# Kernel tuning notes

Hardware: AMD Instinct MI355X
Metric: run time of the kernel (lower is better)

## Reference

```python
import jax, jax.numpy as jnp
import numpy as np

N_HEADS = 4
HEAD_DIM = 128
FMAP_H, FMAP_W = 32, 32
IN_DIM = 512
BATCH = 16


def setup_inputs() -> dict:
    key = jax.random.key(0)
    k1, k2, k3, k4 = jax.random.split(key, 4)
    scale = HEAD_DIM ** (-0.5)
    x = jax.random.normal(k1, (BATCH, IN_DIM, FMAP_H, FMAP_W), dtype=jnp.float32)
    # 1x1 conv weight producing q,k,v stacked along output channels
    conv_w = jax.random.normal(k2, (3 * N_HEADS * HEAD_DIM, IN_DIM), dtype=jnp.float32) * (IN_DIM ** -0.5)
    pos_h = jax.random.normal(k3, (FMAP_H, HEAD_DIM), dtype=jnp.float32) * scale
    pos_w = jax.random.normal(k4, (FMAP_W, HEAD_DIM), dtype=jnp.float32) * scale
    return {"x": x, "conv_w": conv_w, "pos_h": pos_h, "pos_w": pos_w}


def reference(x, conv_w, pos_h, pos_w):
    B, C, H, W = x.shape
    hw = H * W
    scale = HEAD_DIM ** (-0.5)
    # 1x1 conv == pointwise linear over channels
    qkv = jnp.einsum('bchw,oc->bohw', x, conv_w)               # [B, 3*nh*hd, H, W]
    qkv = qkv.reshape(B, 3, N_HEADS, HEAD_DIM, hw)             # chunk + per-head split
    q = jnp.swapaxes(qkv[:, 0], -1, -2) * scale                # [B, nh, hw, hd]
    k = jnp.swapaxes(qkv[:, 1], -1, -2)
    v = jnp.swapaxes(qkv[:, 2], -1, -2)
    # absolute positional embedding: h[i,:]+w[j,:] flattened over positions
    emb = (pos_h[:, None, :] + pos_w[None, :, :]).reshape(hw, HEAD_DIM)
    sim = jnp.einsum('bhid,bhjd->bhij', q, k) + jnp.einsum('bhid,jd->bhij', q, emb)
    attn = jax.nn.softmax(sim, axis=-1)
    out = jnp.einsum('bhij,bhjd->bhid', attn, v)               # [B, nh, hw, hd]
    out = jnp.swapaxes(out, -1, -2)                            # [B, nh, hd, hw]
    return out.reshape(B, N_HEADS * HEAD_DIM, hw // N_HEADS, N_HEADS)
```

## Files before the change

### kernel.cpp

```cpp
#include <hip/hip_runtime.h>

#define NB 16
#define NH 4
#define HD 128
#define HW 1024
#define CIN 512

typedef short s16x8 __attribute__((ext_vector_type(8)));
typedef short s16x4 __attribute__((ext_vector_type(4)));
typedef float f32x4 __attribute__((ext_vector_type(4)));

static __device__ __forceinline__ short f2bf(float f) {
    union { float f; unsigned u; } v; v.f = f;
    unsigned r = v.u + 0x7fffu + ((v.u >> 16) & 1u);
    return (short)(r >> 16);
}

__global__ __launch_bounds__(256) void prep_xw(
    const float* __restrict__ x, const float* __restrict__ w,
    short* __restrict__ xT, short* __restrict__ Wb)
{
    int blk = blockIdx.x;
    if (blk < NB * 16 * 32) {
        int b = blk >> 9, rem = blk & 511;
        int ct = rem >> 5, pt = rem & 31;
        __shared__ float tile[32][33];
        int tc = threadIdx.x >> 5;
        int tp = threadIdx.x & 31;
        const float* xb = x + ((size_t)b * CIN + ct * 32) * HW + pt * 32;
        #pragma unroll
        for (int i = 0; i < 4; i++)
            tile[tc + i * 8][tp] = xb[(size_t)(tc + i * 8) * HW + tp];
        __syncthreads();
        int p = threadIdx.x >> 3, cq = threadIdx.x & 7;
        short* xo = xT + ((size_t)b * HW + pt * 32 + p) * CIN + ct * 32 + cq * 4;
        s16x4 o4 = { f2bf(tile[cq * 4 + 0][p]), f2bf(tile[cq * 4 + 1][p]),
                     f2bf(tile[cq * 4 + 2][p]), f2bf(tile[cq * 4 + 3][p]) };
        *reinterpret_cast<s16x4*>(xo) = o4;
    } else {
        int wb = blk - NB * 16 * 32;
        size_t base = (size_t)wb * 1024 + threadIdx.x * 4;
        const float4 v = *reinterpret_cast<const float4*>(w + base);
        s16x4 o4 = { f2bf(v.x), f2bf(v.y), f2bf(v.z), f2bf(v.w) };
        *reinterpret_cast<s16x4*>(Wb + base) = o4;
    }
}

__global__ __launch_bounds__(256, 3) void qkv_proj(
    const short* __restrict__ xT, const short* __restrict__ Wb,
    const float* __restrict__ pos_h, const float* __restrict__ pos_w,
    short* __restrict__ Q, short* __restrict__ Kp, short* __restrict__ Vt)
{
    __shared__ __align__(16) char smem[34816];
    short* As = (short*)smem;
    short* Bs = As + 128 * 64;
    short* vb = (short*)smem;

    const int pt = blockIdx.x, ot = blockIdx.y, b = blockIdx.z;
    const int tid = threadIdx.x;
    const int wave = tid >> 6, lane = tid & 63;
    const int l16 = lane & 15, quad = lane >> 4;
    const int wm = (wave & 1) * 64, wn = (wave >> 1) * 64;
    const int o0 = ot * 128, p0 = pt * 128;

    const short* xb = xT + (size_t)b * HW * CIN;

    const int r0 = tid >> 3, c0 = tid & 7;
    const int sphys = c0 ^ (r0 & 7);
    const short* wp = Wb + (size_t)(o0 + r0) * CIN + c0 * 8;
    const short* xp = xb + (size_t)(p0 + r0) * CIN + c0 * 8;
    short* adst = As + r0 * 64 + sphys * 8;
    short* bdst = Bs + r0 * 64 + sphys * 8;

    f32x4 acc[4][4];
    #pragma unroll
    for (int i = 0; i < 4; i++)
        #pragma unroll
        for (int j = 0; j < 4; j++)
            acc[i][j] = f32x4{0.f, 0.f, 0.f, 0.f};

    s16x8 wreg[4], xreg[4];
    #pragma unroll
    for (int p = 0; p < 4; p++) {
        wreg[p] = *(const s16x8*)(wp + (size_t)(p * 32) * CIN);
        xreg[p] = *(const s16x8*)(xp + (size_t)(p * 32) * CIN);
    }

    #pragma unroll 1
    for (int kc = 0; kc < CIN; kc += 64) {
        #pragma unroll
        for (int p = 0; p < 4; p++) {
            *(s16x8*)(adst + p * 32 * 64) = wreg[p];
            *(s16x8*)(bdst + p * 32 * 64) = xreg[p];
        }
        __syncthreads();
        int kcn = (kc + 64) & (CIN - 1);
        #pragma unroll
        for (int p = 0; p < 4; p++) {
            wreg[p] = *(const s16x8*)(wp + kcn + (size_t)(p * 32) * CIN);
            xreg[p] = *(const s16x8*)(xp + kcn + (size_t)(p * 32) * CIN);
        }
        #pragma unroll
        for (int kk = 0; kk < 2; kk++) {
            s16x8 aF[4], bF[4];
            #pragma unroll
            for (int mi = 0; mi < 4; mi++)
                aF[mi] = *(const s16x8*)(As + (wm + mi * 16 + l16) * 64
                                         + (((kk * 4 + quad) ^ (l16 & 7)) * 8));
            #pragma unroll
            for (int ni = 0; ni < 4; ni++)
                bF[ni] = *(const s16x8*)(Bs + (wn + ni * 16 + l16) * 64
                                         + (((kk * 4 + quad) ^ (l16 & 7)) * 8));
            #pragma unroll
            for (int mi = 0; mi < 4; mi++)
                #pragma unroll
                for (int ni = 0; ni < 4; ni++)
                    acc[mi][ni] = __builtin_amdgcn_mfma_f32_16x16x32_bf16(
                        aF[mi], bF[ni], acc[mi][ni], 0, 0, 0);
        }
        __syncthreads();
    }

    const int s = ot >> 2, h = ot & 3;
    const size_t bh = (size_t)(b * NH + h);

    if (s == 0) {
        const float qs = 0.08838834764831845f * 1.4426950408889634f;
        short* Qb = Q + bh * (size_t)(HW * HD);
        #pragma unroll
        for (int mi = 0; mi < 4; mi++) {
            int d0 = wm + mi * 16 + quad * 4;
            #pragma unroll
            for (int ni = 0; ni < 4; ni++) {
                int p = p0 + wn + ni * 16 + l16;
                f32x4 a = acc[mi][ni];
                s16x4 o4 = { f2bf(a.x * qs), f2bf(a.y * qs),
                             f2bf(a.z * qs), f2bf(a.w * qs) };
                *reinterpret_cast<s16x4*>(Qb + (size_t)p * HD + d0) = o4;
            }
        }
    } else if (s == 1) {
        short* Kb = Kp + bh * (size_t)(HW * HD);
        #pragma unroll
        for (int mi = 0; mi < 4; mi++) {
            int d0 = wm + mi * 16 + quad * 4;
            #pragma unroll
            for (int ni = 0; ni < 4; ni++) {
                int p = p0 + wn + ni * 16 + l16;
                const float4 eh = *reinterpret_cast<const float4*>(pos_h + (p >> 5) * HD + d0);
                const float4 ew = *reinterpret_cast<const float4*>(pos_w + (p & 31) * HD + d0);
                f32x4 a = acc[mi][ni];
                s16x4 o4 = { f2bf(a.x + eh.x + ew.x), f2bf(a.y + eh.y + ew.y),
                             f2bf(a.z + eh.z + ew.z), f2bf(a.w + eh.w + ew.w) };
                *reinterpret_cast<s16x4*>(Kb + (size_t)p * HD + d0) = o4;
            }
        }
    } else {
        __syncthreads();
        #pragma unroll
        for (int mi = 0; mi < 4; mi++) {
            int d0 = wm + mi * 16 + quad * 4;
            #pragma unroll
            for (int ni = 0; ni < 4; ni++) {
                int p = wn + ni * 16 + l16;
                f32x4 a = acc[mi][ni];
                vb[(d0 + 0) * 136 + p] = f2bf(a.x);
                vb[(d0 + 1) * 136 + p] = f2bf(a.y);
                vb[(d0 + 2) * 136 + p] = f2bf(a.z);
                vb[(d0 + 3) * 136 + p] = f2bf(a.w);
            }
        }
        __syncthreads();
        short* Vb = Vt + bh * (size_t)(HD * HW);
        int d = tid >> 1, half = tid & 1;
        #pragma unroll
        for (int j = 0; j < 8; j++) {
            s16x8 v8 = *(const s16x8*)(vb + d * 136 + half * 64 + j * 8);
            *reinterpret_cast<s16x8*>(Vb + (size_t)d * HW + p0 + half * 64 + j * 8) = v8;
        }
    }
}

__global__ __launch_bounds__(256, 2) void attn_fused(
    const short* __restrict__ Q, const short* __restrict__ Kp,
    const short* __restrict__ Vt, float* __restrict__ out)
{
    __shared__ short Ks[64 * 128];
    __shared__ short Vs[128 * 64];
    __shared__ short Ps[4 * 32 * 64];

    const int flat = blockIdx.x;
    const int qt = flat >> 6;
    const int bh = flat & 63;
    const int tid = threadIdx.x;
    const int wave = tid >> 6, lane = tid & 63;
    const int l16 = lane & 15, quad = lane >> 4;

    const short* Qb = Q + (size_t)bh * (HW * HD);
    const short* Kb = Kp + (size_t)bh * (HW * HD);
    const short* Vb = Vt + (size_t)bh * (HD * HW);
    short* myP = Ps + wave * (32 * 64);

    const int q0 = qt * 128 + wave * 32;

    s16x8 bQ[2][4];
    #pragma unroll
    for (int nt = 0; nt < 2; nt++)
        #pragma unroll
        for (int kk = 0; kk < 4; kk++)
            bQ[nt][kk] = *(const s16x8*)(Qb + (size_t)(q0 + nt * 16 + l16) * HD
                                         + kk * 32 + quad * 8);

    s16x8 ones;
    #pragma unroll
    for (int j = 0; j < 8; j++) ones[j] = (short)0x3F80;

    f32x4 Oacc[2][8];
    #pragma unroll
    for (int mt = 0; mt < 2; mt++)
        #pragma unroll
        for (int dt = 0; dt < 8; dt++)
            Oacc[mt][dt] = f32x4{0.f, 0.f, 0.f, 0.f};
    f32x4 lacc[2] = { f32x4{0.f, 0.f, 0.f, 0.f}, f32x4{0.f, 0.f, 0.f, 0.f} };

    const int kKey = tid >> 4, kC = tid & 15;
    const int kPhys = kC ^ kKey;
    const short* kgp = Kb + (size_t)kKey * HD + kC * 8;
    short* kdst = Ks + kKey * 128 + kPhys * 8;
    const int vD = tid >> 3, vC = tid & 7;
    const int vPhys = vC ^ (vD & 7);
    const short* vgp = Vb + (size_t)vD * HW + vC * 8;
    short* vdst = Vs + vD * 64 + vPhys * 8;

    s16x8 kreg[4], vreg[4];
    #pragma unroll
    for (int i = 0; i < 4; i++) {
        kreg[i] = *(const s16x8*)(kgp + (size_t)(i * 16) * HD);
        vreg[i] = *(const s16x8*)(vgp + (size_t)(i * 32) * HW);
    }

    #pragma unroll 1
    for (int kt = 0; kt < 16; kt++) {
        #pragma unroll
        for (int i = 0; i < 4; i++) {
            *(s16x8*)(kdst + i * 16 * 128) = kreg[i];
            *(s16x8*)(vdst + i * 32 * 64) = vreg[i];
        }
        __syncthreads();

        int ktn = (kt + 1) & 15;
        #pragma unroll
        for (int i = 0; i < 4; i++) {
            kreg[i] = *(const s16x8*)(kgp + (size_t)(ktn * 64 + i * 16) * HD);
            vreg[i] = *(const s16x8*)(vgp + ktn * 64 + (size_t)(i * 32) * HW);
        }

        f32x4 c[4][2];
        #pragma unroll
        for (int mtp = 0; mtp < 4; mtp++) {
            s16x8 aK[4];
            #pragma unroll
            for (int kk = 0; kk < 4; kk++)
                aK[kk] = *(const s16x8*)(Ks + (mtp * 16 + l16) * 128
                                         + (((kk * 4 + quad) ^ l16) * 8));
            c[mtp][0] = f32x4{0.f, 0.f, 0.f, 0.f};
            c[mtp][1] = f32x4{0.f, 0.f, 0.f, 0.f};
            #pragma unroll
            for (int kk = 0; kk < 4; kk++) {
                c[mtp][0] = __builtin_amdgcn_mfma_f32_16x16x32_bf16(
                    aK[kk], bQ[0][kk], c[mtp][0], 0, 0, 0);
                c[mtp][1] = __builtin_amdgcn_mfma_f32_16x16x32_bf16(
                    aK[kk], bQ[1][kk], c[mtp][1], 0, 0, 0);
            }
        }

        #pragma unroll
        for (int mtp = 0; mtp < 4; mtp++)
            #pragma unroll
            for (int nt = 0; nt < 2; nt++) {
                f32x4 pv = c[mtp][nt];
                s16x4 pp = { f2bf(__builtin_amdgcn_exp2f(pv[0])),
                             f2bf(__builtin_amdgcn_exp2f(pv[1])),
                             f2bf(__builtin_amdgcn_exp2f(pv[2])),
                             f2bf(__builtin_amdgcn_exp2f(pv[3])) };
                int q = nt * 16 + l16;
                int chunk = 2 * mtp + (quad >> 1);
                int phys = chunk ^ (l16 & 7);
                *(s16x4*)(myP + q * 64 + phys * 8 + (quad & 1) * 4) = pp;
            }

        s16x8 aP[2][2];
        #pragma unroll
        for (int mt = 0; mt < 2; mt++)
            #pragma unroll
            for (int kp = 0; kp < 2; kp++) {
                int phys = (kp * 4 + quad) ^ (l16 & 7);
                aP[mt][kp] = *(const s16x8*)(myP + (mt * 16 + l16) * 64 + phys * 8);
            }

        #pragma unroll
        for (int mt = 0; mt < 2; mt++)
            #pragma unroll
            for (int kp = 0; kp < 2; kp++)
                lacc[mt] = __builtin_amdgcn_mfma_f32_16x16x32_bf16(
                    aP[mt][kp], ones, lacc[mt], 0, 0, 0);

        #pragma unroll
        for (int dt = 0; dt < 8; dt++) {
            s16x8 bV0 = *(const s16x8*)(Vs + (dt * 16 + l16) * 64
                                        + ((quad ^ (l16 & 7)) * 8));
            s16x8 bV1 = *(const s16x8*)(Vs + (dt * 16 + l16) * 64
                                        + (((4 + quad) ^ (l16 & 7)) * 8));
            #pragma unroll
            for (int mt = 0; mt < 2; mt++) {
                Oacc[mt][dt] = __builtin_amdgcn_mfma_f32_16x16x32_bf16(
                    aP[mt][0], bV0, Oacc[mt][dt], 0, 0, 0);
                Oacc[mt][dt] = __builtin_amdgcn_mfma_f32_16x16x32_bf16(
                    aP[mt][1], bV1, Oacc[mt][dt], 0, 0, 0);
            }
        }
        __syncthreads();
    }

    float* ob = out + (size_t)bh * (HD * HW);
    #pragma unroll
    for (int mt = 0; mt < 2; mt++) {
        float inv[4];
        #pragma unroll
        for (int r = 0; r < 4; r++) inv[r] = __builtin_amdgcn_rcpf(lacc[mt][r]);
        int prow = q0 + mt * 16 + quad * 4;
        #pragma unroll
        for (int dt = 0; dt < 8; dt++) {
            int d = dt * 16 + l16;
            f32x4 o = Oacc[mt][dt];
            float4 o4 = { o[0] * inv[0], o[1] * inv[1],
                          o[2] * inv[2], o[3] * inv[3] };
            *reinterpret_cast<float4*>(ob + (size_t)d * HW + prow) = o4;
        }
    }
}

extern "C" void kernel_launch(void* const* d_in, const int* in_sizes, int n_in,
                              void* d_out, int out_size, void* d_ws, size_t ws_size,
                              hipStream_t stream) {
    const float* x  = (const float*)d_in[0];
    const float* w  = (const float*)d_in[1];
    const float* ph = (const float*)d_in[2];
    const float* pw = (const float*)d_in[3];

    const size_t BHPD = (size_t)NB * NH * HW * HD;
    short* Q    = (short*)d_ws;
    short* Kp   = Q + BHPD;
    short* Vt   = Kp + BHPD;
    short* xT   = Vt + BHPD;
    short* Wb   = xT + (size_t)NB * HW * CIN;
    float* outp = (float*)d_out;

    prep_xw<<<dim3(NB * 16 * 32 + 768), 256, 0, stream>>>(x, w, xT, Wb);
    qkv_proj<<<dim3(8, 12, NB), 256, 0, stream>>>(xT, Wb, ph, pw, Q, Kp, Vt);
    attn_fused<<<dim3(512), 256, 0, stream>>>(Q, Kp, Vt, outp);
}
```

Baseline: 168.4 us.

## Double-buffer K/V tiles in LDS and split P@V into halves

Allocates two LDS buffers for K and V so the next tile is written while the current one is consumed, which drops one of the two barriers per iteration and prefetches two tiles ahead. The P tile is now staged in two 32-key halves using a smaller padded buffer, so exp/convert and the P@V MFMAs interleave. s_setprio raises priority around the MFMA sections. LDS use roughly doubles for K/V, which may cut occupancy from the 2 blocks per CU requested by launch bounds.

```diff
diff --git a/kernel.cpp b/kernel.cpp
--- a/kernel.cpp
+++ b/kernel.cpp
@@ -185,9 +185,9 @@
     const short* __restrict__ Q, const short* __restrict__ Kp,
     const short* __restrict__ Vt, float* __restrict__ out)
 {
-    __shared__ short Ks[64 * 128];
-    __shared__ short Vs[128 * 64];
-    __shared__ short Ps[4 * 32 * 64];
+    __shared__ __align__(16) short Ks[2][64 * 128];
+    __shared__ __align__(16) short Vs[2][128 * 64];
+    __shared__ __align__(16) short Ps[4][32 * 40];
 
     const int flat = blockIdx.x;
     const int qt = flat >> 6;
@@ -199,7 +199,7 @@
     const short* Qb = Q + (size_t)bh * (HW * HD);
     const short* Kb = Kp + (size_t)bh * (HW * HD);
     const short* Vb = Vt + (size_t)bh * (HD * HW);
-    short* myP = Ps + wave * (32 * 64);
+    short* myP = Ps[wave];
 
     const int q0 = qt * 128 + wave * 32;
 
@@ -226,11 +226,11 @@
     const int kKey = tid >> 4, kC = tid & 15;
     const int kPhys = kC ^ kKey;
     const short* kgp = Kb + (size_t)kKey * HD + kC * 8;
-    short* kdst = Ks + kKey * 128 + kPhys * 8;
+    const int kOff = kKey * 128 + kPhys * 8;
     const int vD = tid >> 3, vC = tid & 7;
     const int vPhys = vC ^ (vD & 7);
     const short* vgp = Vb + (size_t)vD * HW + vC * 8;
-    short* vdst = Vs + vD * 64 + vPhys * 8;
+    const int vOff = vD * 64 + vPhys * 8;
 
     s16x8 kreg[4], vreg[4];
     #pragma unroll
@@ -238,17 +238,30 @@
         kreg[i] = *(const s16x8*)(kgp + (size_t)(i * 16) * HD);
         vreg[i] = *(const s16x8*)(vgp + (size_t)(i * 32) * HW);
     }
+    #pragma unroll
+    for (int i = 0; i < 4; i++) {
+        *(s16x8*)(&Ks[0][kOff] + i * 16 * 128) = kreg[i];
+        *(s16x8*)(&Vs[0][vOff] + i * 32 * 64) = vreg[i];
+    }
+    #pragma unroll
+    for (int i = 0; i < 4; i++) {
+        kreg[i] = *(const s16x8*)(kgp + (size_t)(64 + i * 16) * HD);
+        vreg[i] = *(const s16x8*)(vgp + 64 + (size_t)(i * 32) * HW);
+    }
+    __syncthreads();
 
     #pragma unroll 1
     for (int kt = 0; kt < 16; kt++) {
+        const int cur = kt & 1, nxt = cur ^ 1;
+        const short* ks = Ks[cur];
+        const short* vs = Vs[cur];
+
         #pragma unroll
         for (int i = 0; i < 4; i++) {
-            *(s16x8*)(kdst + i * 16 * 128) = kreg[i];
-            *(s16x8*)(vdst + i * 32 * 64) = vreg[i];
-        }
-        __syncthreads();
-
-        int ktn = (kt + 1) & 15;
+            *(s16x8*)(&Ks[nxt][kOff] + i * 16 * 128) = kreg[i];
+            *(s16x8*)(&Vs[nxt][vOff] + i * 32 * 64) = vreg[i];
+        }
+        int ktn = (kt + 2) & 15;
         #pragma unroll
         for (int i = 0; i < 4; i++) {
             kreg[i] = *(const s16x8*)(kgp + (size_t)(ktn * 64 + i * 16) * HD);
@@ -256,12 +269,13 @@
         }
 
         f32x4 c[4][2];
+        __builtin_amdgcn_s_setprio(1);
         #pragma unroll
         for (int mtp = 0; mtp < 4; mtp++) {
             s16x8 aK[4];
             #pragma unroll
             for (int kk = 0; kk < 4; kk++)
-                aK[kk] = *(const s16x8*)(Ks + (mtp * 16 + l16) * 128
+                aK[kk] = *(const s16x8*)(ks + (mtp * 16 + l16) * 128
                                          + (((kk * 4 + quad) ^ l16) * 8));
             c[mtp][0] = f32x4{0.f, 0.f, 0.f, 0.f};
             c[mtp][1] = f32x4{0.f, 0.f, 0.f, 0.f};
@@ -273,51 +287,44 @@
                     aK[kk], bQ[1][kk], c[mtp][1], 0, 0, 0);
             }
         }
-
-        #pragma unroll
-        for (int mtp = 0; mtp < 4; mtp++)
-            #pragma unroll
-            for (int nt = 0; nt < 2; nt++) {
-                f32x4 pv = c[mtp][nt];
-                s16x4 pp = { f2bf(__builtin_amdgcn_exp2f(pv[0])),
-                             f2bf(__builtin_amdgcn_exp2f(pv[1])),
-                             f2bf(__builtin_amdgcn_exp2f(pv[2])),
-                             f2bf(__builtin_amdgcn_exp2f(pv[3])) };
-                int q = nt * 16 + l16;
-                int chunk = 2 * mtp + (quad >> 1);
-                int phys = chunk ^ (l16 & 7);
-                *(s16x4*)(myP + q * 64 + phys * 8 + (quad & 1) * 4) = pp;
-            }
-
-        s16x8 aP[2][2];
-        #pragma unroll
-        for (int mt = 0; mt < 2; mt++)
-            #pragma unroll
-            for (int kp = 0; kp < 2; kp++) {
-                int phys = (kp * 4 + quad) ^ (l16 & 7);
-                aP[mt][kp] = *(const s16x8*)(myP + (mt * 16 + l16) * 64 + phys * 8);
-            }
-
-        #pragma unroll
-        for (int mt = 0; mt < 2; mt++)
-            #pragma unroll
-            for (int kp = 0; kp < 2; kp++)
+        __builtin_amdgcn_s_setprio(0);
+
+        #pragma unroll
+        for (int h = 0; h < 2; h++) {
+            #pragma unroll
+            for (int m2 = 0; m2 < 2; m2++)
+                #pragma unroll
+                for (int nt = 0; nt < 2; nt++) {
+                    f32x4 pv = c[h * 2 + m2][nt];
+                    s16x4 pp = { f2bf(__builtin_amdgcn_exp2f(pv[0])),
+                                 f2bf(__builtin_amdgcn_exp2f(pv[1])),
+                                 f2bf(__builtin_amdgcn_exp2f(pv[2])),
+                                 f2bf(__builtin_amdgcn_exp2f(pv[3])) };
+                    int q = nt * 16 + l16;
+                    *(s16x4*)(myP + q * 40 + m2 * 16 + quad * 4) = pp;
+                }
+
+            s16x8 aP[2];
+            #pragma unroll
+            for (int mt = 0; mt < 2; mt++)
+                aP[mt] = *(const s16x8*)(myP + (mt * 16 + l16) * 40 + quad * 8);
+
+            __builtin_amdgcn_s_setprio(1);
+            #pragma unroll
+            for (int mt = 0; mt < 2; mt++)
                 lacc[mt] = __builtin_amdgcn_mfma_f32_16x16x32_bf16(
-                    aP[mt][kp], ones, lacc[mt], 0, 0, 0);
-
-        #pragma unroll
-        for (int dt = 0; dt < 8; dt++) {
-            s16x8 bV0 = *(const s16x8*)(Vs + (dt * 16 + l16) * 64
-                                        + ((quad ^ (l16 & 7)) * 8));
-            s16x8 bV1 = *(const s16x8*)(Vs + (dt * 16 + l16) * 64
-                                        + (((4 + quad) ^ (l16 & 7)) * 8));
-            #pragma unroll
-            for (int mt = 0; mt < 2; mt++) {
-                Oacc[mt][dt] = __builtin_amdgcn_mfma_f32_16x16x32_bf16(
-                    aP[mt][0], bV0, Oacc[mt][dt], 0, 0, 0);
-                Oacc[mt][dt] = __builtin_amdgcn_mfma_f32_16x16x32_bf16(
-                    aP[mt][1], bV1, Oacc[mt][dt], 0, 0, 0);
-            }
+                    aP[mt], ones, lacc[mt], 0, 0, 0);
+
+            #pragma unroll
+            for (int dt = 0; dt < 8; dt++) {
+                s16x8 bV = *(const s16x8*)(vs + (dt * 16 + l16) * 64
+                                           + (((h * 4 + quad) ^ (l16 & 7)) * 8));
+                #pragma unroll
+                for (int mt = 0; mt < 2; mt++)
+                    Oacc[mt][dt] = __builtin_amdgcn_mfma_f32_16x16x32_bf16(
+                        aP[mt], bV, Oacc[mt][dt], 0, 0, 0);
+            }
+            __builtin_amdgcn_s_setprio(0);
         }
         __syncthreads();
     }
```

Measured after the change: 175.5 us. 1.04x slower.
